# Performance work log

Measured on AMD Instinct MI355X. Metric: run time of the kernel, lower is better.

Reference implementation:

```python
import jax, jax.numpy as jnp
import numpy as np

N_COMP = 16  # sedenion components

def _cd_table(n):
    """Cayley-Dickson basis multiplication table: e_i * e_j = sign[i,j] * e_{idx[i,j]}."""
    if n == 1:
        return np.array([[1]], dtype=np.int64), np.array([[0]], dtype=np.int64)
    m = n // 2
    s, k = _cd_table(m)
    conj = np.where(np.arange(m) == 0, 1, -1)  # conj(e_0)=e_0, conj(e_i)=-e_i
    S = np.zeros((n, n), dtype=np.int64)
    K = np.zeros((n, n), dtype=np.int64)
    for i in range(n):
        for j in range(n):
            if i < m and j < m:          # (a,0)(c,0) = (ac, 0)
                S[i, j] = s[i, j]; K[i, j] = k[i, j]
            elif i < m:                  # (a,0)(0,d) = (0, d a)
                q = j - m
                S[i, j] = s[q, i]; K[i, j] = m + k[q, i]
            elif j < m:                  # (0,b)(c,0) = (0, b c*)
                p = i - m
                S[i, j] = s[p, j] * conj[j]; K[i, j] = m + k[p, j]
            else:                        # (0,b)(0,d) = (-d* b, 0)
                p, q = i - m, j - m
                S[i, j] = -conj[q] * s[q, p]; K[i, j] = k[q, p]
    return S, K

SIGN, IDX = _cd_table(N_COMP)

def _sedenion_kernel(w_comp):
    """Assemble the (16n, 16n) real matrix of the sedenion linear map from 16 (n,n) component weights."""
    blocks = [[None] * N_COMP for _ in range(N_COMP)]
    for i in range(N_COMP):
        for j in range(N_COMP):
            blocks[j][int(IDX[i, j])] = float(SIGN[i, j]) * w_comp[i]
    return jnp.concatenate([jnp.concatenate(row, axis=1) for row in blocks], axis=0)


def setup_inputs() -> dict:
    key = jax.random.key(0)
    k1, k2, k3, k4 = jax.random.split(key, 4)
    B, C, H, W = 8, 96, 256, 256
    x = jax.random.normal(k1, (B, C, H, W), jnp.float32)
    w_comp = jax.random.normal(k2, (N_COMP, C, C), jnp.float32) * 0.02
    proj_w = jax.random.normal(k3, (C, C), jnp.float32) * 0.02
    proj_b = jax.random.normal(k4, (C,), jnp.float32) * 0.02
    return {"x": x, "w_comp": w_comp, "proj_w": proj_w, "proj_b": proj_b}


def reference(x, w_comp, proj_w, proj_b):
    B, C, H, W = x.shape
    h, w = H // 4, W // 4
    # get_window: 'b c (h s1) (w s2) -> b h w (s1 s2 c)' with s1=s2=4
    xw = x.reshape(B, C, h, 4, w, 4).transpose(0, 2, 4, 3, 5, 1).reshape(B, h, w, 16 * C)
    big = _sedenion_kernel(w_comp)          # (16C, 16C)
    y = xw @ big                            # sedenion linear on windowed features
    # reverse_window + 'b c h w -> b h w c' fused: (B,h,w,16C) -> (B,H,W,C)
    y = y.reshape(B, h, w, 4, 4, C).transpose(0, 1, 3, 2, 4, 5).reshape(B, H, W, C)
    y = jax.nn.gelu(y, approximate=False)   # nn.GELU (exact); dropouts are identity (p=0)
    y = y @ proj_w.T + proj_b               # nn.Linear(dim, dim)
    return y.transpose(0, 3, 1, 2)          # 'b h w c -> b c h w'
```

## Files before the change

kernel.cpp:

```cpp
#include <hip/hip_runtime.h>
#include <hip/hip_bf16.h>

typedef __attribute__((ext_vector_type(8))) short short8v;
typedef __attribute__((ext_vector_type(4))) float float4v;

struct SedTab { signed char sgn[256]; signed char idx[256]; };

__device__ inline unsigned short f2bf(float f) {
    __hip_bfloat16 h = __float2bfloat16(f);
    return *reinterpret_cast<unsigned short*>(&h);
}
__device__ inline float bf2f(unsigned short u) {
    union { unsigned int i; float f; } x; x.i = ((unsigned)u) << 16; return x.f;
}

#define GLOAD_LDS16(g, l) __builtin_amdgcn_global_load_lds( \
    (const __attribute__((address_space(1))) void*)(g), \
    (__attribute__((address_space(3))) void*)(l), 16, 0, 0)

#define VMCNT(n) asm volatile("s_waitcnt vmcnt(" #n ")" ::: "memory")

__global__ __launch_bounds__(256) void build_bigT(
    const float* __restrict__ w_comp, unsigned short* __restrict__ bigT, SedTab tab)
{
    int e = blockIdx.x * 256 + threadIdx.x;
    if (e >= 1536 * 1536) return;
    int n = e / 1536, k = e - n * 1536;
    int t_out = n / 96, c = n - t_out * 96;
    int t_in = k / 96, m = k - t_in * 96;
    int i = tab.idx[t_in * 16 + t_out];
    float s = (float)tab.sgn[t_in * 16 + t_out];
    float v = s * w_comp[(i * 96 + m) * 96 + c];
    bigT[e] = f2bf(v);
}

__global__ __launch_bounds__(256) void window_cast(
    const float* __restrict__ x, unsigned short* __restrict__ xw)
{
    __shared__ unsigned short lds[96][260];
    int blk = blockIdx.x;
    int s1 = blk & 3, hh = (blk >> 2) & 63, b = blk >> 8;
    const float* src = x + (size_t)b * 6291456 + (size_t)(4 * hh + s1) * 256;

    for (int i = threadIdx.x; i < 6144; i += 256) {
        int m = i >> 6;
        int q = (i & 63) << 2;
        float4 v = *(const float4*)(src + (size_t)m * 65536 + q);
        lds[m][q + 0] = f2bf(v.x);
        lds[m][q + 1] = f2bf(v.y);
        lds[m][q + 2] = f2bf(v.z);
        lds[m][q + 3] = f2bf(v.w);
    }
    __syncthreads();
    size_t rowbase = (size_t)((b * 64 + hh) * 64) * 1536 + (size_t)s1 * 384;
    for (int i = threadIdx.x; i < 3072; i += 256) {
        int ww = i / 48, g = i - ww * 48;
        int s2 = g / 12, mg = (g - s2 * 12) * 8;
        int qq = 4 * ww + s2;
        short8v pk;
        #pragma unroll
        for (int j = 0; j < 8; ++j) pk[j] = (short)lds[mg + j][qq];
        *(short8v*)(xw + rowbase + (size_t)ww * 1536 + s2 * 96 + mg) = pk;
    }
}

__global__ __launch_bounds__(512, 2) void gemm_sed8(
    const unsigned short* __restrict__ A,
    const unsigned short* __restrict__ Bt,
    unsigned short* __restrict__ Yg)
{
    __shared__ unsigned short As[3][128 * 64];
    __shared__ unsigned short Bs[3][256 * 64];
    const int t = threadIdx.x;
    const int lane = t & 63, w = t >> 6;
    const int wm = w >> 2, wn = w & 3;
    const int lr = lane & 15, lg = lane >> 4;

    const int bid = blockIdx.x;
    const int wg = (bid & 7) * 192 + (bid >> 3);
    const int nt = wg >> 8, mt = wg & 255;
    const int m0 = mt * 128, n0 = nt * 256;

    float4v acc[4][4];
    #pragma unroll
    for (int i = 0; i < 4; ++i)
        #pragma unroll
        for (int j = 0; j < 4; ++j) acc[i][j] = (float4v)0.0f;

    auto stageA = [&](int kt, int slot, int i) {
        const int c = t + i * 512;
        const int row = c >> 3;
        const int kc = (((c & 7) ^ (row & 7)) << 3);
        GLOAD_LDS16(A + (size_t)(m0 + row) * 1536 + kt * 64 + kc,
                    (char*)&As[slot][0] + c * 16);
    };
    auto stageB = [&](int kt, int slot, int i) {
        const int c = t + i * 512;
        const int row = c >> 3;
        const int kc = (((c & 7) ^ (row & 7)) << 3);
        GLOAD_LDS16(Bt + (size_t)(n0 + row) * 1536 + kt * 64 + kc,
                    (char*)&Bs[slot][0] + c * 16);
    };

    stageA(0, 0, 0); stageA(0, 0, 1);
    stageB(0, 0, 0); stageB(0, 0, 1); stageB(0, 0, 2); stageB(0, 0, 3);
    stageA(1, 1, 0); stageA(1, 1, 1);
    stageB(1, 1, 0); stageB(1, 1, 1); stageB(1, 1, 2); stageB(1, 1, 3);
    VMCNT(6);
    __builtin_amdgcn_s_barrier();

    int slot = 0;
    for (int kt = 0; kt < 24; ++kt) {
        const int ps = (slot == 0) ? 2 : slot - 1;
        const int pf = kt + 2;
        const bool st = (pf < 24);

        short8v a[4][2], b0[2][2];
        #pragma unroll
        for (int mf = 0; mf < 4; ++mf)
            #pragma unroll
            for (int ks = 0; ks < 2; ++ks) {
                const int row = wm * 64 + mf * 16 + lr;
                const int col = (ks * 32 + lg * 8) ^ ((row & 7) << 3);
                a[mf][ks] = *(const short8v*)(&As[slot][row * 64 + col]);
            }
        #pragma unroll
        for (int nf = 0; nf < 2; ++nf)
            #pragma unroll
            for (int ks = 0; ks < 2; ++ks) {
                const int row = wn * 64 + nf * 16 + lr;
                const int col = (ks * 32 + lg * 8) ^ ((row & 7) << 3);
                b0[nf][ks] = *(const short8v*)(&Bs[slot][row * 64 + col]);
            }
        if (st) { stageA(pf, ps, 0); stageA(pf, ps, 1); stageB(pf, ps, 0); }
        __builtin_amdgcn_s_barrier();
        __builtin_amdgcn_s_setprio(1);
        #pragma unroll
        for (int ks = 0; ks < 2; ++ks)
            #pragma unroll
            for (int mf = 0; mf < 4; ++mf)
                #pragma unroll
                for (int nf = 0; nf < 2; ++nf)
                    acc[mf][nf] = __builtin_amdgcn_mfma_f32_16x16x32_bf16(
                        a[mf][ks], b0[nf][ks], acc[mf][nf], 0, 0, 0);
        __builtin_amdgcn_s_setprio(0);
        __builtin_amdgcn_s_barrier();

        short8v b1[2][2];
        #pragma unroll
        for (int nf = 0; nf < 2; ++nf)
            #pragma unroll
            for (int ks = 0; ks < 2; ++ks) {
                const int row = wn * 64 + (nf + 2) * 16 + lr;
                const int col = (ks * 32 + lg * 8) ^ ((row & 7) << 3);
                b1[nf][ks] = *(const short8v*)(&Bs[slot][row * 64 + col]);
            }
        if (st) { stageB(pf, ps, 1); stageB(pf, ps, 2); stageB(pf, ps, 3); }
        if (kt < 22)       { VMCNT(6); }
        else if (kt == 22) { VMCNT(0); }
        __builtin_amdgcn_s_barrier();
        __builtin_amdgcn_s_setprio(1);
        #pragma unroll
        for (int ks = 0; ks < 2; ++ks)
            #pragma unroll
            for (int mf = 0; mf < 4; ++mf)
                #pragma unroll
                for (int nf = 0; nf < 2; ++nf)
                    acc[mf][nf + 2] = __builtin_amdgcn_mfma_f32_16x16x32_bf16(
                        a[mf][ks], b1[nf][ks], acc[mf][nf + 2], 0, 0, 0);
        __builtin_amdgcn_s_setprio(0);
        __builtin_amdgcn_s_barrier();

        slot = (slot == 2) ? 0 : slot + 1;
    }

    #pragma unroll
    for (int mf = 0; mf < 4; ++mf) {
        #pragma unroll
        for (int r = 0; r < 4; ++r) {
            const int gm = m0 + wm * 64 + mf * 16 + lg * 4 + r;
            #pragma unroll
            for (int nf = 0; nf < 4; ++nf) {
                const int gn = n0 + wn * 64 + nf * 16 + lr;
                float v = acc[mf][nf][r];
                float g = 0.5f * v * (1.0f + erff(v * 0.70710678118654752f));
                Yg[(size_t)gm * 1536 + gn] = f2bf(g);
            }
        }
    }
}

__global__ __launch_bounds__(256, 2) void proj_mfma(
    const unsigned short* __restrict__ Yg,
    const float* __restrict__ pw, const float* __restrict__ pb,
    float* __restrict__ out)
{
    __shared__ unsigned short gys[256 * 104];
    __shared__ unsigned short pws[96 * 104];
    __shared__ float pbs[96];

    const int blk = blockIdx.x;
    const int s1 = blk & 3, hh = (blk >> 2) & 63, b = blk >> 8;
    const int t = threadIdx.x;
    const int lane = t & 63, w = t >> 6;
    const int lr = lane & 15;

    for (int i = t; i < 9216; i += 256) {
        int r = i / 96, c = i - r * 96;
        pws[r * 104 + c] = f2bf(pw[i]);
    }
    if (t < 96) pbs[t] = pb[t];

    size_t rowbase = (size_t)((b * 64 + hh) * 64) * 1536 + (size_t)s1 * 384;
    for (int i = t; i < 3072; i += 256) {
        int ww = i / 48, v = i - ww * 48;
        short8v pk = *(const short8v*)(Yg + rowbase + (size_t)ww * 1536 + v * 8);
        int s2 = v / 12;
        int c = (v - s2 * 12) * 8;
        int q = 4 * ww + s2;
        *(short8v*)(&gys[q * 104 + c]) = pk;
    }
    __syncthreads();

    float4v acc[6][4];
    #pragma unroll
    for (int i = 0; i < 6; ++i)
        #pragma unroll
        for (int j = 0; j < 4; ++j) acc[i][j] = (float4v)0.0f;

    #pragma unroll
    for (int ks = 0; ks < 3; ++ks) {
        const int lk = ks * 32 + ((lane >> 4) << 3);
        short8v af[6], bf[4];
        #pragma unroll
        for (int mf = 0; mf < 6; ++mf)
            af[mf] = *(const short8v*)(&pws[(mf * 16 + lr) * 104 + lk]);
        #pragma unroll
        for (int nf = 0; nf < 4; ++nf)
            bf[nf] = *(const short8v*)(&gys[(w * 64 + nf * 16 + lr) * 104 + lk]);
        #pragma unroll
        for (int mf = 0; mf < 6; ++mf)
            #pragma unroll
            for (int nf = 0; nf < 4; ++nf)
                acc[mf][nf] = __builtin_amdgcn_mfma_f32_16x16x32_bf16(
                    af[mf], bf[nf], acc[mf][nf], 0, 0, 0);
    }

    const int p = 4 * hh + s1;
    const size_t obase = (size_t)b * 6291456 + (size_t)p * 256;
    #pragma unroll
    for (int mf = 0; mf < 6; ++mf) {
        #pragma unroll
        for (int r = 0; r < 4; ++r) {
            const int c = mf * 16 + (lane >> 4) * 4 + r;
            const float bias = pbs[c];
            #pragma unroll
            for (int nf = 0; nf < 4; ++nf) {
                const int q = w * 64 + nf * 16 + lr;
                out[obase + (size_t)c * 65536 + q] = acc[mf][nf][r] + bias;
            }
        }
    }
}

static void cd_table(int n, int* S, int* K) {
    if (n == 1) { S[0] = 1; K[0] = 0; return; }
    int m = n / 2;
    int s[64], k[64];
    cd_table(m, s, k);
    for (int i = 0; i < n; ++i) {
        for (int j = 0; j < n; ++j) {
            if (i < m && j < m) { S[i*n+j] = s[i*m+j]; K[i*n+j] = k[i*m+j]; }
            else if (i < m) { int q = j - m; S[i*n+j] = s[q*m+i]; K[i*n+j] = m + k[q*m+i]; }
            else if (j < m) { int p = i - m; int cj = (j == 0) ? 1 : -1;
                              S[i*n+j] = s[p*m+j] * cj; K[i*n+j] = m + k[p*m+j]; }
            else { int p = i - m, q = j - m; int cq = (q == 0) ? 1 : -1;
                   S[i*n+j] = -cq * s[q*m+p]; K[i*n+j] = k[q*m+p]; }
        }
    }
}

extern "C" void kernel_launch(void* const* d_in, const int* in_sizes, int n_in,
                              void* d_out, int out_size, void* d_ws, size_t ws_size,
                              hipStream_t stream) {
    const float* x      = (const float*)d_in[0];
    const float* w_comp = (const float*)d_in[1];
    const float* proj_w = (const float*)d_in[2];
    const float* proj_b = (const float*)d_in[3];
    float* out = (float*)d_out;

    unsigned short* BigT = (unsigned short*)d_ws;
    unsigned short* Yg   = (unsigned short*)((char*)d_ws + 4718592);
    unsigned short* Xw   = (unsigned short*)d_out;

    int S16[256], K16[256];
    cd_table(16, S16, K16);
    SedTab tab;
    for (int i = 0; i < 16; ++i)
        for (int j = 0; j < 16; ++j) {
            int k = K16[i * 16 + j];
            tab.idx[j * 16 + k] = (signed char)i;
            tab.sgn[j * 16 + k] = (signed char)S16[i * 16 + j];
        }

    hipLaunchKernelGGL(build_bigT, dim3(9216), dim3(256), 0, stream, w_comp, BigT, tab);
    hipLaunchKernelGGL(window_cast, dim3(2048), dim3(256), 0, stream, x, Xw);
    hipLaunchKernelGGL(gemm_sed8, dim3(1536), dim3(512), 0, stream, Xw, BigT, Yg);
    hipLaunchKernelGGL(proj_mfma, dim3(2048), dim3(256), 0, stream, Yg, proj_w, proj_b, out);
}
```

Measured before the change: 364.5 us.

## Enlarge GEMM tile to 256x256 with four-phase MFMA/prefetch schedule

Doubles the M tile of the main sedenion GEMM from 128 to 256 rows, so each workgroup computes a 256x256 output block and the grid halves. A is triple-buffered and B double-buffered in LDS. Each k-step is split into four MFMA phases interleaved with staged global-to-LDS prefetches. The aim is more arithmetic per byte loaded and less global/LDS traffic per MFMA. In exchange, accumulator registers double and LDS use grows to 160KB, which will likely drop occupancy to one block per CU despite launch_bounds(512,2), and the tail wave gets coarser.

```diff
diff --git a/kernel.cpp b/kernel.cpp
--- a/kernel.cpp
+++ b/kernel.cpp
@@ -69,116 +69,132 @@
     const unsigned short* __restrict__ Bt,
     unsigned short* __restrict__ Yg)
 {
-    __shared__ unsigned short As[3][128 * 64];
-    __shared__ unsigned short Bs[3][256 * 64];
+    __shared__ unsigned short As[3][256 * 64];
+    __shared__ unsigned short Bs[2][256 * 64];
     const int t = threadIdx.x;
     const int lane = t & 63, w = t >> 6;
     const int wm = w >> 2, wn = w & 3;
     const int lr = lane & 15, lg = lane >> 4;
 
     const int bid = blockIdx.x;
-    const int wg = (bid & 7) * 192 + (bid >> 3);
-    const int nt = wg >> 8, mt = wg & 255;
-    const int m0 = mt * 128, n0 = nt * 256;
-
-    float4v acc[4][4];
-    #pragma unroll
-    for (int i = 0; i < 4; ++i)
+    const int wg = (bid & 7) * 96 + (bid >> 3);
+    const int nt = wg >> 7, mt = wg & 127;
+    const int m0 = mt * 256, n0 = nt * 256;
+
+    float4v acc[8][4];
+    #pragma unroll
+    for (int i = 0; i < 8; ++i)
         #pragma unroll
         for (int j = 0; j < 4; ++j) acc[i][j] = (float4v)0.0f;
 
-    auto stageA = [&](int kt, int slot, int i) {
+    auto stageA = [&](int kt, int half, int i) {
         const int c = t + i * 512;
-        const int row = c >> 3;
-        const int kc = (((c & 7) ^ (row & 7)) << 3);
+        const int row = half * 128 + (c >> 3);
+        const int kc = ((c & 7) ^ (row & 7)) << 3;
         GLOAD_LDS16(A + (size_t)(m0 + row) * 1536 + kt * 64 + kc,
-                    (char*)&As[slot][0] + c * 16);
+                    (char*)&As[kt % 3][0] + half * 16384 + c * 16);
     };
-    auto stageB = [&](int kt, int slot, int i) {
+    auto stageB = [&](int kt, int half, int i) {
         const int c = t + i * 512;
-        const int row = c >> 3;
-        const int kc = (((c & 7) ^ (row & 7)) << 3);
+        const int row = half * 128 + (c >> 3);
+        const int kc = ((c & 7) ^ (row & 7)) << 3;
         GLOAD_LDS16(Bt + (size_t)(n0 + row) * 1536 + kt * 64 + kc,
-                    (char*)&Bs[slot][0] + c * 16);
+                    (char*)&Bs[kt & 1][0] + half * 16384 + c * 16);
     };
 
-    stageA(0, 0, 0); stageA(0, 0, 1);
-    stageB(0, 0, 0); stageB(0, 0, 1); stageB(0, 0, 2); stageB(0, 0, 3);
-    stageA(1, 1, 0); stageA(1, 1, 1);
-    stageB(1, 1, 0); stageB(1, 1, 1); stageB(1, 1, 2); stageB(1, 1, 3);
-    VMCNT(6);
+    stageA(0, 0, 0); stageA(0, 0, 1); stageA(0, 1, 0); stageA(0, 1, 1);
+    stageB(0, 0, 0); stageB(0, 0, 1); stageB(0, 1, 0); stageB(0, 1, 1);
+    stageA(1, 0, 0); stageA(1, 0, 1); stageA(1, 1, 0); stageA(1, 1, 1);
+    VMCNT(4);
     __builtin_amdgcn_s_barrier();
 
-    int slot = 0;
+    const int c0 = (lg * 8) ^ ((lr & 7) << 3);
+    const int c1 = (32 + lg * 8) ^ ((lr & 7) << 3);
+
     for (int kt = 0; kt < 24; ++kt) {
-        const int ps = (slot == 0) ? 2 : slot - 1;
-        const int pf = kt + 2;
-        const bool st = (pf < 24);
-
-        short8v a[4][2], b0[2][2];
-        #pragma unroll
-        for (int mf = 0; mf < 4; ++mf)
-            #pragma unroll
-            for (int ks = 0; ks < 2; ++ks) {
-                const int row = wm * 64 + mf * 16 + lr;
-                const int col = (ks * 32 + lg * 8) ^ ((row & 7) << 3);
-                a[mf][ks] = *(const short8v*)(&As[slot][row * 64 + col]);
-            }
-        #pragma unroll
-        for (int nf = 0; nf < 2; ++nf)
-            #pragma unroll
-            for (int ks = 0; ks < 2; ++ks) {
-                const int row = wn * 64 + nf * 16 + lr;
-                const int col = (ks * 32 + lg * 8) ^ ((row & 7) << 3);
-                b0[nf][ks] = *(const short8v*)(&Bs[slot][row * 64 + col]);
-            }
-        if (st) { stageA(pf, ps, 0); stageA(pf, ps, 1); stageB(pf, ps, 0); }
+        const unsigned short* as = &As[kt % 3][0];
+        const unsigned short* bs = &Bs[kt & 1][0];
+        const int arow0 = wm * 128 + lr;
+        const int brow0 = wn * 64 + lr;
+
+        short8v a0[4], b0[4];
+        #pragma unroll
+        for (int mf = 0; mf < 4; ++mf)
+            a0[mf] = *(const short8v*)(as + (arow0 + mf * 16) * 64 + c0);
+        #pragma unroll
+        for (int nf = 0; nf < 4; ++nf)
+            b0[nf] = *(const short8v*)(bs + (brow0 + nf * 16) * 64 + c0);
+        if (kt < 23) { stageB(kt + 1, 0, 0); stageB(kt + 1, 0, 1); }
         __builtin_amdgcn_s_barrier();
         __builtin_amdgcn_s_setprio(1);
         #pragma unroll
-        for (int ks = 0; ks < 2; ++ks)
-            #pragma unroll
-            for (int mf = 0; mf < 4; ++mf)
-                #pragma unroll
-                for (int nf = 0; nf < 2; ++nf)
-                    acc[mf][nf] = __builtin_amdgcn_mfma_f32_16x16x32_bf16(
-                        a[mf][ks], b0[nf][ks], acc[mf][nf], 0, 0, 0);
+        for (int mf = 0; mf < 4; ++mf)
+            #pragma unroll
+            for (int nf = 0; nf < 4; ++nf)
+                acc[mf][nf] = __builtin_amdgcn_mfma_f32_16x16x32_bf16(
+                    a0[mf], b0[nf], acc[mf][nf], 0, 0, 0);
         __builtin_amdgcn_s_setprio(0);
         __builtin_amdgcn_s_barrier();
 
-        short8v b1[2][2];
-        #pragma unroll
-        for (int nf = 0; nf < 2; ++nf)
-            #pragma unroll
-            for (int ks = 0; ks < 2; ++ks) {
-                const int row = wn * 64 + (nf + 2) * 16 + lr;
-                const int col = (ks * 32 + lg * 8) ^ ((row & 7) << 3);
-                b1[nf][ks] = *(const short8v*)(&Bs[slot][row * 64 + col]);
-            }
-        if (st) { stageB(pf, ps, 1); stageB(pf, ps, 2); stageB(pf, ps, 3); }
-        if (kt < 22)       { VMCNT(6); }
+        short8v a1[4];
+        #pragma unroll
+        for (int mf = 0; mf < 4; ++mf)
+            a1[mf] = *(const short8v*)(as + (arow0 + 64 + mf * 16) * 64 + c0);
+        if (kt < 23) { stageB(kt + 1, 1, 0); stageB(kt + 1, 1, 1); }
+        __builtin_amdgcn_s_barrier();
+        __builtin_amdgcn_s_setprio(1);
+        #pragma unroll
+        for (int mf = 0; mf < 4; ++mf)
+            #pragma unroll
+            for (int nf = 0; nf < 4; ++nf)
+                acc[4 + mf][nf] = __builtin_amdgcn_mfma_f32_16x16x32_bf16(
+                    a1[mf], b0[nf], acc[4 + mf][nf], 0, 0, 0);
+        __builtin_amdgcn_s_setprio(0);
+        __builtin_amdgcn_s_barrier();
+
+        short8v a2[4], b1[4];
+        #pragma unroll
+        for (int mf = 0; mf < 4; ++mf)
+            a2[mf] = *(const short8v*)(as + (arow0 + mf * 16) * 64 + c1);
+        #pragma unroll
+        for (int nf = 0; nf < 4; ++nf)
+            b1[nf] = *(const short8v*)(bs + (brow0 + nf * 16) * 64 + c1);
+        if (kt < 22) { stageA(kt + 2, 0, 0); stageA(kt + 2, 0, 1); }
+        __builtin_amdgcn_s_barrier();
+        __builtin_amdgcn_s_setprio(1);
+        #pragma unroll
+        for (int mf = 0; mf < 4; ++mf)
+            #pragma unroll
+            for (int nf = 0; nf < 4; ++nf)
+                acc[mf][nf] = __builtin_amdgcn_mfma_f32_16x16x32_bf16(
+                    a2[mf], b1[nf], acc[mf][nf], 0, 0, 0);
+        __builtin_amdgcn_s_setprio(0);
+        __builtin_amdgcn_s_barrier();
+
+        short8v a3[4];
+        #pragma unroll
+        for (int mf = 0; mf < 4; ++mf)
+            a3[mf] = *(const short8v*)(as + (arow0 + 64 + mf * 16) * 64 + c1);
+        if (kt < 22) { stageA(kt + 2, 1, 0); stageA(kt + 2, 1, 1); }
+        __builtin_amdgcn_s_barrier();
+        __builtin_amdgcn_s_setprio(1);
+        #pragma unroll
+        for (int mf = 0; mf < 4; ++mf)
+            #pragma unroll
+            for (int nf = 0; nf < 4; ++nf)
+                acc[4 + mf][nf] = __builtin_amdgcn_mfma_f32_16x16x32_bf16(
+                    a3[mf], b1[nf], acc[4 + mf][nf], 0, 0, 0);
+        __builtin_amdgcn_s_setprio(0);
+        if (kt < 22)       { VMCNT(4); }
         else if (kt == 22) { VMCNT(0); }
         __builtin_amdgcn_s_barrier();
-        __builtin_amdgcn_s_setprio(1);
-        #pragma unroll
-        for (int ks = 0; ks < 2; ++ks)
-            #pragma unroll
-            for (int mf = 0; mf < 4; ++mf)
-                #pragma unroll
-                for (int nf = 0; nf < 2; ++nf)
-                    acc[mf][nf + 2] = __builtin_amdgcn_mfma_f32_16x16x32_bf16(
-                        a[mf][ks], b1[nf][ks], acc[mf][nf + 2], 0, 0, 0);
-        __builtin_amdgcn_s_setprio(0);
-        __builtin_amdgcn_s_barrier();
-
-        slot = (slot == 2) ? 0 : slot + 1;
-    }
-
-    #pragma unroll
-    for (int mf = 0; mf < 4; ++mf) {
+    }
+
+    #pragma unroll
+    for (int mf = 0; mf < 8; ++mf) {
         #pragma unroll
         for (int r = 0; r < 4; ++r) {
-            const int gm = m0 + wm * 64 + mf * 16 + lg * 4 + r;
+            const int gm = m0 + wm * 128 + mf * 16 + lg * 4 + r;
             #pragma unroll
             for (int nf = 0; nf < 4; ++nf) {
                 const int gn = n0 + wn * 64 + nf * 16 + lr;
@@ -305,6 +321,6 @@
 
     hipLaunchKernelGGL(build_bigT, dim3(9216), dim3(256), 0, stream, w_comp, BigT, tab);
     hipLaunchKernelGGL(window_cast, dim3(2048), dim3(256), 0, stream, x, Xw);
-    hipLaunchKernelGGL(gemm_sed8, dim3(1536), dim3(512), 0, stream, Xw, BigT, Yg);
+    hipLaunchKernelGGL(gemm_sed8, dim3(768), dim3(512), 0, stream, Xw, BigT, Yg);
     hipLaunchKernelGGL(proj_mfma, dim3(2048), dim3(256), 0, stream, Yg, proj_w, proj_b, out);
 }
```

New measurement: 347.4 us. 1.05x faster.
